# Performance work log

Hardware: AMD Instinct MI355X
Metric: run time of the kernel (lower is better)

The kernel has to match this reference:

```python
import jax, jax.numpy as jnp
import numpy as np

N, E = 100000, 1000000
IN_F, HID, OUT, K = 64, 64, 32, 3


def setup_inputs() -> dict:
    key = jax.random.key(0)
    ks = jax.random.split(key, 8)
    s = 0.05
    return {
        "features": jax.random.normal(ks[0], (N, IN_F), dtype=jnp.float32),
        "src": jax.random.randint(ks[1], (E,), 0, N),
        "dst": jax.random.randint(ks[2], (E,), 0, N),
        "n_nodes": N,
        "W1": jax.random.normal(ks[3], (K * IN_F, HID), jnp.float32) * s,
        "b1": jnp.zeros((HID,), jnp.float32),
        "W2": jax.random.normal(ks[4], (K * HID, HID), jnp.float32) * s,
        "b2": jnp.zeros((HID,), jnp.float32),
        "Wm1": jax.random.normal(ks[5], (HID, HID), jnp.float32) * s,
        "bm1": jnp.zeros((HID,), jnp.float32),
        "Wm2": jax.random.normal(ks[6], (HID, OUT), jnp.float32) * s,
        "bm2": jnp.zeros((OUT,), jnp.float32),
    }


def _cheb_conv(x, src, dst, dinv, W, b, n_nodes, k=K):
    # DGL ChebConv with lambda_max = 2 (re_norm = 2/lambda_max = 1).
    def prop(h):  # D^{-1/2} A D^{-1/2} h via edge gather/scatter
        m = (h * dinv)[src]                                   # [E, F]
        agg = jax.ops.segment_sum(m, dst, num_segments=n_nodes)
        return agg * dinv

    X0 = x
    Xs = [X0]
    X1 = -prop(X0)                 # -re_norm*L h + (re_norm-1)*X0, re_norm=1
    Xs.append(X1)
    for _ in range(2, k):
        Xi = -2.0 * prop(X1) - X0  # Chebyshev recursion
        Xs.append(Xi)
        X0, X1 = X1, Xi
    return jnp.concatenate(Xs, axis=1) @ W + b  # Linear(k*F_in -> F_out)


def reference(features, src, dst, n_nodes, W1, b1, W2, b2, Wm1, bm1, Wm2, bm2):
    deg = jax.ops.segment_sum(
        jnp.ones((src.shape[0],), dtype=features.dtype), dst, num_segments=n_nodes
    )
    dinv = (jnp.clip(deg, 1.0, None) ** -0.5)[:, None]  # in-degree^{-1/2}
    x = jax.nn.relu(_cheb_conv(features, src, dst, dinv, W1, b1, n_nodes))
    x = jax.nn.relu(_cheb_conv(x, src, dst, dinv, W2, b2, n_nodes))
    return jax.nn.relu(x @ Wm1 + bm1) @ Wm2 + bm2
```

## Files before the change

### kernel.cpp

```cpp
#include <hip/hip_runtime.h>


typedef unsigned short ushort_t;
typedef __attribute__((ext_vector_type(8))) short v8s;
typedef __attribute__((ext_vector_type(4))) float v4f;

__device__ inline ushort_t f2bf(float f) {
    unsigned u = __float_as_uint(f);
    return (ushort_t)((u + 0x7FFFu + ((u >> 16) & 1u)) >> 16);
}
__device__ inline float bf2f(ushort_t h) {
    return __uint_as_float(((unsigned)h) << 16);
}

#define BSH 9
#define BSZ (1 << BSH)
#define CHUNK 4096

__global__ void k_wprep(const float* __restrict__ W1, const float* __restrict__ W2,
                        const float* __restrict__ Wm1, const float* __restrict__ Wm2,
                        ushort_t* __restrict__ W1t, ushort_t* __restrict__ W2t,
                        ushort_t* __restrict__ Wm1t, ushort_t* __restrict__ Wm2t,
                        int* __restrict__ gbase, int* __restrict__ done, int NB) {
    int i = blockIdx.x * 256 + threadIdx.x;
    if (i < 12288) { int k = i >> 6, n = i & 63; W1t[n * 192 + k] = f2bf(W1[i]); return; }
    i -= 12288;
    if (i < 12288) { int k = i >> 6, n = i & 63; W2t[n * 192 + k] = f2bf(W2[i]); return; }
    i -= 12288;
    if (i < 4096) { int k = i >> 6, n = i & 63; Wm1t[n * 64 + k] = f2bf(Wm1[i]); return; }
    i -= 4096;
    if (i < 2048) { int k = i >> 5, n = i & 31; Wm2t[n * 64 + k] = f2bf(Wm2[i]); return; }
    i -= 2048;
    if (i < NB) gbase[i] = 0;
    if (i == NB) *done = 0;
}

__global__ __launch_bounds__(256) void k_bhist(const int* __restrict__ dst,
                                               int* __restrict__ gbase,
                                               int* __restrict__ gcur,
                                               int* __restrict__ done, int E, int NB) {
    __shared__ int h[1024];
    __shared__ int isLast;
    for (int i = threadIdx.x; i < NB; i += 256) h[i] = 0;
    __syncthreads();
    for (int i = blockIdx.x * blockDim.x + threadIdx.x; i < E; i += gridDim.x * blockDim.x)
        atomicAdd(&h[dst[i] >> BSH], 1);
    __syncthreads();
    for (int i = threadIdx.x; i < NB; i += 256)
        if (h[i]) atomicAdd(&gbase[i], h[i]);
    __threadfence();
    __syncthreads();
    if (threadIdx.x == 0) isLast = (atomicAdd(done, 1) == (int)gridDim.x - 1);
    __syncthreads();
    if (isLast) {
        __threadfence();
        int t = threadIdx.x;
        int v = (t < NB) ? gbase[t] : 0;
        h[t] = v;
        __syncthreads();
        for (int off = 1; off < 256; off <<= 1) {
            int u = (t >= off) ? h[t - off] : 0;
            __syncthreads();
            h[t] += u;
            __syncthreads();
        }
        if (t < NB) {
            int excl = h[t] - v;
            gbase[t] = excl;
            gcur[t] = excl;
        }
    }
}

__global__ __launch_bounds__(256) void k_bucket2(
    const int* __restrict__ src, const int* __restrict__ dst,
    int* __restrict__ gcur, int2* __restrict__ eb, int E, int NB) {
    __shared__ int ls[CHUNK];
    __shared__ int ld[CHUNK];
    __shared__ int hist[1024];
    __shared__ int bbase[1024];
    int t = threadIdx.x;
    int base = blockIdx.x * CHUNK;
    int count = E - base;
    if (count > CHUNK) count = CHUNK;
    for (int i = t; i < NB; i += 256) hist[i] = 0;
    __syncthreads();
    for (int i = t; i < count; i += 256) {
        int s = src[base + i];
        int d = dst[base + i];
        ls[i] = s;
        ld[i] = d;
        atomicAdd(&hist[d >> BSH], 1);
    }
    __syncthreads();
    for (int b = t; b < NB; b += 256) {
        int c = hist[b];
        bbase[b] = c ? atomicAdd(&gcur[b], c) : 0;
        hist[b] = 0;
    }
    __syncthreads();
    for (int i = t; i < count; i += 256) {
        int d = ld[i];
        int b = d >> BSH;
        int off = atomicAdd(&hist[b], 1);
        eb[bbase[b] + off] = make_int2(ls[i], d);
    }
}

__global__ __launch_bounds__(256) void k_local(
    const int2* __restrict__ eb, const int* __restrict__ gbase,
    int* __restrict__ col, int* __restrict__ row_ptr,
    float* __restrict__ dinv, int N, int E, int NB) {
    __shared__ int cnt[BSZ];
    __shared__ int tsum[256];
    int t = threadIdx.x;
    int b = blockIdx.x;
    int d0 = b << BSH;
    cnt[2 * t] = 0;
    cnt[2 * t + 1] = 0;
    __syncthreads();
    int beg = gbase[b];
    int end = (b + 1 < NB) ? gbase[b + 1] : E;
    for (int i = beg + t; i < end; i += 256)
        atomicAdd(&cnt[eb[i].y - d0], 1);
    __syncthreads();
    int c0 = cnt[2 * t], c1 = cnt[2 * t + 1];
    int mysum = c0 + c1;
    tsum[t] = mysum;
    __syncthreads();
    for (int off = 1; off < 256; off <<= 1) {
        int u = 0;
        if (t >= off) u = tsum[t - off];
        __syncthreads();
        tsum[t] += u;
        __syncthreads();
    }
    int rbase = beg + tsum[t] - mysum;
    int d = d0 + 2 * t;
    if (d < N) {
        row_ptr[d] = rbase;
        dinv[d] = rsqrtf(fmaxf((float)c0, 1.0f));
    }
    if (d + 1 < N) {
        row_ptr[d + 1] = rbase + c0;
        dinv[d + 1] = rsqrtf(fmaxf((float)c1, 1.0f));
    }
    cnt[2 * t] = rbase;
    cnt[2 * t + 1] = rbase + c0;
    __syncthreads();
    for (int i = beg + t; i < end; i += 256) {
        int2 e = eb[i];
        int p = atomicAdd(&cnt[e.y - d0], 1);
        col[p] = e.x;
    }
    if (b == NB - 1 && t == 0) row_ptr[N] = E;
}

__global__ void k_tobf16(const float4* __restrict__ X, const float* __restrict__ dinv,
                         ushort4* __restrict__ Y, int n4) {
    int i = blockIdx.x * blockDim.x + threadIdx.x;
    if (i < n4) {
        float s = dinv[i >> 4];
        float4 v = X[i];
        ushort4 o;
        o.x = f2bf(v.x * s); o.y = f2bf(v.y * s); o.z = f2bf(v.z * s); o.w = f2bf(v.w * s);
        Y[i] = o;
    }
}

__device__ inline float4 gather_sum(const ushort_t* __restrict__ Xb,
                                    const int* __restrict__ col,
                                    int beg, int end, int g, int fl) {
    float4 a0 = make_float4(0.f, 0.f, 0.f, 0.f);
    float4 a1 = make_float4(0.f, 0.f, 0.f, 0.f);
    int e = beg + g;
    for (; e + 4 < end; e += 8) {
        int s0 = col[e], s1 = col[e + 4];
        ushort4 u0 = *(const ushort4*)&Xb[(size_t)s0 * 64 + fl];
        ushort4 u1 = *(const ushort4*)&Xb[(size_t)s1 * 64 + fl];
        a0.x += bf2f(u0.x); a0.y += bf2f(u0.y); a0.z += bf2f(u0.z); a0.w += bf2f(u0.w);
        a1.x += bf2f(u1.x); a1.y += bf2f(u1.y); a1.z += bf2f(u1.z); a1.w += bf2f(u1.w);
    }
    if (e < end) {
        int s0 = col[e];
        ushort4 u0 = *(const ushort4*)&Xb[(size_t)s0 * 64 + fl];
        a0.x += bf2f(u0.x); a0.y += bf2f(u0.y); a0.z += bf2f(u0.z); a0.w += bf2f(u0.w);
    }
    float4 acc;
    acc.x = a0.x + a1.x; acc.y = a0.y + a1.y;
    acc.z = a0.z + a1.z; acc.w = a0.w + a1.w;
    acc.x += __shfl_xor(acc.x, 16); acc.y += __shfl_xor(acc.y, 16);
    acc.z += __shfl_xor(acc.z, 16); acc.w += __shfl_xor(acc.w, 16);
    acc.x += __shfl_xor(acc.x, 32); acc.y += __shfl_xor(acc.y, 32);
    acc.z += __shfl_xor(acc.z, 32); acc.w += __shfl_xor(acc.w, 32);
    return acc;
}

template <int MODE>
__global__ __launch_bounds__(256) void k_prop(
    const ushort_t* __restrict__ Xb, const int* __restrict__ rp,
    const int* __restrict__ col, const float* __restrict__ dinv,
    const ushort_t* __restrict__ X0b, ushort_t* __restrict__ OUTB, int N) {
    int wid = (blockIdx.x * blockDim.x + threadIdx.x) >> 6;
    int lane = threadIdx.x & 63;
    if (wid >= N) return;
    int g = lane >> 4;
    int fl = (lane & 15) * 4;
    int beg = rp[wid], end = rp[wid + 1];
    float4 a0 = make_float4(0.f, 0.f, 0.f, 0.f);
    float4 a1 = make_float4(0.f, 0.f, 0.f, 0.f);
    int e = beg + g;
    for (; e + 4 < end; e += 8) {
        int s0 = col[e], s1 = col[e + 4];
        ushort4 u0 = *(const ushort4*)&Xb[(size_t)s0 * 64 + fl];
        ushort4 u1 = *(const ushort4*)&Xb[(size_t)s1 * 64 + fl];
        a0.x += bf2f(u0.x); a0.y += bf2f(u0.y); a0.z += bf2f(u0.z); a0.w += bf2f(u0.w);
        a1.x += bf2f(u1.x); a1.y += bf2f(u1.y); a1.z += bf2f(u1.z); a1.w += bf2f(u1.w);
    }
    if (e < end) {
        int s0 = col[e];
        ushort4 u0 = *(const ushort4*)&Xb[(size_t)s0 * 64 + fl];
        a0.x += bf2f(u0.x); a0.y += bf2f(u0.y); a0.z += bf2f(u0.z); a0.w += bf2f(u0.w);
    }
    float4 acc;
    acc.x = a0.x + a1.x;
    acc.y = a0.y + a1.y;
    acc.z = a0.z + a1.z;
    acc.w = a0.w + a1.w;
    acc.x += __shfl_xor(acc.x, 16);
    acc.y += __shfl_xor(acc.y, 16);
    acc.z += __shfl_xor(acc.z, 16);
    acc.w += __shfl_xor(acc.w, 16);
    acc.x += __shfl_xor(acc.x, 32);
    acc.y += __shfl_xor(acc.y, 32);
    acc.z += __shfl_xor(acc.z, 32);
    acc.w += __shfl_xor(acc.w, 32);
    if (g == 0) {
        float di = dinv[wid];
        ushort4 ob;
        if (MODE == 1) {
            float m = -di * di;
            ob.x = f2bf(m * acc.x);
            ob.y = f2bf(m * acc.y);
            ob.z = f2bf(m * acc.z);
            ob.w = f2bf(m * acc.w);
        } else {
            ushort4 x0u = *(const ushort4*)&X0b[(size_t)wid * 64 + fl];
            float m = -2.0f * di;
            float rd = 1.0f / di;
            ob.x = f2bf(fmaf(m, acc.x, -rd * bf2f(x0u.x)));
            ob.y = f2bf(fmaf(m, acc.y, -rd * bf2f(x0u.y)));
            ob.z = f2bf(fmaf(m, acc.z, -rd * bf2f(x0u.z)));
            ob.w = f2bf(fmaf(m, acc.w, -rd * bf2f(x0u.w)));
        }
        *(ushort4*)&OUTB[(size_t)wid * 64 + fl] = ob;
    }
}

__global__ __launch_bounds__(512, 8) void k_pc1(
    const ushort_t* __restrict__ Xb, const int* __restrict__ rp,
    const int* __restrict__ col, const float* __restrict__ dinv,
    const ushort_t* __restrict__ T0, const ushort_t* __restrict__ Wt,
    const float* __restrict__ b, ushort_t* __restrict__ Yb, int N) {
    __shared__ ushort_t XA[64][72];
    int tid = threadIdx.x;
    int w = tid >> 6, lane = tid & 63;
    int g = lane >> 4, fl = (lane & 15) * 4;
    int node0 = blockIdx.x * 64;

    for (int i = 0; i < 8; i++) {
        int nd = node0 + w * 8 + i;
        ushort4 ob;
        ob.x = 0; ob.y = 0; ob.z = 0; ob.w = 0;
        if (nd < N) {
            float4 acc = gather_sum(Xb, col, rp[nd], rp[nd + 1], g, fl);
            if (g == 0) {
                float di = dinv[nd];
                ushort4 x0u = *(const ushort4*)&T0[(size_t)nd * 64 + fl];
                float m = -2.0f * di;
                float rd = 1.0f / di;
                ob.x = f2bf(fmaf(m, acc.x, -rd * bf2f(x0u.x)));
                ob.y = f2bf(fmaf(m, acc.y, -rd * bf2f(x0u.y)));
                ob.z = f2bf(fmaf(m, acc.z, -rd * bf2f(x0u.z)));
                ob.w = f2bf(fmaf(m, acc.w, -rd * bf2f(x0u.w)));
            }
        }
        if (g == 0) *(ushort4*)&XA[w * 8 + i][fl] = ob;
    }
    __syncthreads();

    int n16 = lane & 15, q = lane >> 4;
    int f = w >> 1, h = w & 1;
    int arow = node0 + f * 16 + n16;

    v4f acc_s[2], acc_u[2];
    acc_s[0] = (v4f){0.f, 0.f, 0.f, 0.f};
    acc_s[1] = (v4f){0.f, 0.f, 0.f, 0.f};
    acc_u[0] = (v4f){0.f, 0.f, 0.f, 0.f};
    acc_u[1] = (v4f){0.f, 0.f, 0.f, 0.f};
#pragma unroll
    for (int ks = 0; ks < 6; ks++) {
        int c = ks >> 1;
        int kk = (ks & 1) * 32 + q * 8;
        v8s av = {0, 0, 0, 0, 0, 0, 0, 0};
        if (c == 2) {
            av = *(const v8s*)&XA[f * 16 + n16][kk];
        } else {
            const ushort_t* P = (c == 0) ? T0 : Xb;
            if (arow < N) av = *(const v8s*)&P[(size_t)arow * 64 + kk];
        }
#pragma unroll
        for (int t2 = 0; t2 < 2; t2++) {
            int t = h * 2 + t2;
            v8s bv = *(const v8s*)&Wt[(size_t)(t * 16 + n16) * 192 + ks * 32 + q * 8];
            if (c < 2)
                acc_s[t2] = __builtin_amdgcn_mfma_f32_16x16x32_bf16(av, bv, acc_s[t2], 0, 0, 0);
            else
                acc_u[t2] = __builtin_amdgcn_mfma_f32_16x16x32_bf16(av, bv, acc_u[t2], 0, 0, 0);
        }
    }
    int rbase = node0 + f * 16 + q * 4;
#pragma unroll
    for (int r = 0; r < 4; r++) {
        int row = rbase + r;
        if (row < N) {
            float dv = dinv[row];
            float rd = 1.0f / dv;
#pragma unroll
            for (int t2 = 0; t2 < 2; t2++) {
                int t = h * 2 + t2;
                float y = fmaf(rd, acc_s[t2][r], acc_u[t2][r]) + b[t * 16 + n16];
                y = fmaxf(y, 0.0f);
                Yb[(size_t)row * 64 + t * 16 + n16] = f2bf(dv * y);
            }
        }
    }
}

__global__ __launch_bounds__(512, 8) void k_pc2(
    const ushort_t* __restrict__ Xb, const int* __restrict__ rp,
    const int* __restrict__ col, const float* __restrict__ dinv,
    const ushort_t* __restrict__ T0, const ushort_t* __restrict__ Wt,
    const float* __restrict__ b,
    const ushort_t* __restrict__ Wm1t, const float* __restrict__ bm1,
    const ushort_t* __restrict__ Wm2t, const float* __restrict__ bm2,
    float* __restrict__ out, int N) {
    __shared__ ushort_t smem[9728];
    ushort_t (*XA)[72] = (ushort_t(*)[72])smem;
    ushort_t (*Hs0)[76] = (ushort_t(*)[76])smem;
    ushort_t (*Hs1)[76] = (ushort_t(*)[76])(smem + 64 * 76);
    int tid = threadIdx.x;
    int w = tid >> 6, lane = tid & 63;
    int g = lane >> 4, fl = (lane & 15) * 4;
    int node0 = blockIdx.x * 64;

    for (int i = 0; i < 8; i++) {
        int nd = node0 + w * 8 + i;
        ushort4 ob;
        ob.x = 0; ob.y = 0; ob.z = 0; ob.w = 0;
        if (nd < N) {
            float4 acc = gather_sum(Xb, col, rp[nd], rp[nd + 1], g, fl);
            if (g == 0) {
                float di = dinv[nd];
                ushort4 x0u = *(const ushort4*)&T0[(size_t)nd * 64 + fl];
                float m = -2.0f * di;
                float rd = 1.0f / di;
                ob.x = f2bf(fmaf(m, acc.x, -rd * bf2f(x0u.x)));
                ob.y = f2bf(fmaf(m, acc.y, -rd * bf2f(x0u.y)));
                ob.z = f2bf(fmaf(m, acc.z, -rd * bf2f(x0u.z)));
                ob.w = f2bf(fmaf(m, acc.w, -rd * bf2f(x0u.w)));
            }
        }
        if (g == 0) *(ushort4*)&XA[w * 8 + i][fl] = ob;
    }
    __syncthreads();

    int n16 = lane & 15, q = lane >> 4;
    int f = w >> 1, h = w & 1;
    int arow = node0 + f * 16 + n16;

    v8s av4 = *(const v8s*)&XA[f * 16 + n16][q * 8];
    v8s av5 = *(const v8s*)&XA[f * 16 + n16][32 + q * 8];
    __syncthreads();

    v4f acc_s[2], acc_u[2];
    acc_s[0] = (v4f){0.f, 0.f, 0.f, 0.f};
    acc_s[1] = (v4f){0.f, 0.f, 0.f, 0.f};
    acc_u[0] = (v4f){0.f, 0.f, 0.f, 0.f};
    acc_u[1] = (v4f){0.f, 0.f, 0.f, 0.f};
#pragma unroll
    for (int ks = 0; ks < 6; ks++) {
        int c = ks >> 1;
        int kk = (ks & 1) * 32 + q * 8;
        v8s av;
        if (c == 2) {
            av = (ks & 1) ? av5 : av4;
        } else {
            const ushort_t* P = (c == 0) ? T0 : Xb;
            av = (v8s){0, 0, 0, 0, 0, 0, 0, 0};
            if (arow < N) av = *(const v8s*)&P[(size_t)arow * 64 + kk];
        }
#pragma unroll
        for (int t2 = 0; t2 < 2; t2++) {
            int t = h * 2 + t2;
            v8s bv = *(const v8s*)&Wt[(size_t)(t * 16 + n16) * 192 + ks * 32 + q * 8];
            if (c < 2)
                acc_s[t2] = __builtin_amdgcn_mfma_f32_16x16x32_bf16(av, bv, acc_s[t2], 0, 0, 0);
            else
                acc_u[t2] = __builtin_amdgcn_mfma_f32_16x16x32_bf16(av, bv, acc_u[t2], 0, 0, 0);
        }
    }
    int lr = f * 16 + q * 4;
    int rbase = node0 + lr;
#pragma unroll
    for (int r = 0; r < 4; r++) {
        int row = rbase + r;
        if (row < N) {
            float dv = dinv[row];
            float rd = 1.0f / dv;
#pragma unroll
            for (int t2 = 0; t2 < 2; t2++) {
                int t = h * 2 + t2;
                float y = fmaf(rd, acc_s[t2][r], acc_u[t2][r]) + b[t * 16 + n16];
                Hs0[lr + r][t * 16 + n16] = f2bf(fmaxf(y, 0.0f));
            }
        } else {
#pragma unroll
            for (int t2 = 0; t2 < 2; t2++)
                Hs0[lr + r][(h * 2 + t2) * 16 + n16] = 0;
        }
    }
    __syncthreads();

    v4f acc[2];
    acc[0] = (v4f){0.f, 0.f, 0.f, 0.f};
    acc[1] = (v4f){0.f, 0.f, 0.f, 0.f};
#pragma unroll
    for (int ks = 0; ks < 2; ks++) {
        v8s av1 = *(const v8s*)&Hs0[f * 16 + n16][ks * 32 + q * 8];
#pragma unroll
        for (int t2 = 0; t2 < 2; t2++) {
            int t = h * 2 + t2;
            v8s bv = *(const v8s*)&Wm1t[(size_t)(t * 16 + n16) * 64 + ks * 32 + q * 8];
            acc[t2] = __builtin_amdgcn_mfma_f32_16x16x32_bf16(av1, bv, acc[t2], 0, 0, 0);
        }
    }
#pragma unroll
    for (int r = 0; r < 4; r++)
#pragma unroll
        for (int t2 = 0; t2 < 2; t2++) {
            int t = h * 2 + t2;
            float y = acc[t2][r] + bm1[t * 16 + n16];
            Hs1[lr + r][t * 16 + n16] = f2bf(fmaxf(y, 0.0f));
        }
    __syncthreads();

    v4f a2 = (v4f){0.f, 0.f, 0.f, 0.f};
#pragma unroll
    for (int ks = 0; ks < 2; ks++) {
        v8s av2 = *(const v8s*)&Hs1[f * 16 + n16][ks * 32 + q * 8];
        v8s bv = *(const v8s*)&Wm2t[(size_t)(h * 16 + n16) * 64 + ks * 32 + q * 8];
        a2 = __builtin_amdgcn_mfma_f32_16x16x32_bf16(av2, bv, a2, 0, 0, 0);
    }
#pragma unroll
    for (int r = 0; r < 4; r++) {
        int row = rbase + r;
        if (row < N)
            out[(size_t)row * 32 + h * 16 + n16] = a2[r] + bm2[h * 16 + n16];
    }
}

extern "C" void kernel_launch(void* const* d_in, const int* in_sizes, int n_in,
                              void* d_out, int out_size, void* d_ws, size_t ws_size,
                              hipStream_t stream) {
    const float* features = (const float*)d_in[0];
    const int* src = (const int*)d_in[1];
    const int* dst = (const int*)d_in[2];
    const float* W1 = (const float*)d_in[4];
    const float* b1 = (const float*)d_in[5];
    const float* W2 = (const float*)d_in[6];
    const float* b2 = (const float*)d_in[7];
    const float* Wm1 = (const float*)d_in[8];
    const float* bm1 = (const float*)d_in[9];
    const float* Wm2 = (const float*)d_in[10];
    const float* bm2 = (const float*)d_in[11];
    float* out = (float*)d_out;

    int N = in_sizes[0] / 64;
    int E = in_sizes[1];
    int NB = (N + BSZ - 1) >> BSH;

    float* ws = (float*)d_ws;
    float* dinv = ws;
    int* row_ptr = (int*)(dinv + N);
    int* gbase = row_ptr + (N + 1);
    int* gcur = gbase + 1024;
    int* done = gcur + 1024;
    int* col = done + 16;
    int2* eb = (int2*)(((uintptr_t)(col + E) + 7) & ~(uintptr_t)7);
    ushort_t* Fb  = (ushort_t*)(eb + E);
    ushort_t* X1b = Fb  + (size_t)N * 64;
    ushort_t* H1b = X1b + (size_t)N * 64;
    ushort_t* W1t = H1b + (size_t)N * 64;
    ushort_t* W2t = W1t + 64 * 192;
    ushort_t* Wm1t = W2t + 64 * 192;
    ushort_t* Wm2t = Wm1t + 64 * 64;

    int pblk = (N * 64 + 255) / 256;
    int gblk = (N + 63) / 64;
    int n4 = N * 16;
    int cblk = (n4 + 255) / 256;
    int bblk = (E + CHUNK - 1) / CHUNK;

    k_wprep<<<(30720 + 1024 + 255) / 256, 256, 0, stream>>>(
        W1, W2, Wm1, Wm2, W1t, W2t, Wm1t, Wm2t, gbase, done, NB);

    k_bhist<<<512, 256, 0, stream>>>(dst, gbase, gcur, done, E, NB);
    k_bucket2<<<bblk, 256, 0, stream>>>(src, dst, gcur, eb, E, NB);
    k_local<<<NB, 256, 0, stream>>>(eb, gbase, col, row_ptr, dinv, N, E, NB);

    k_tobf16<<<cblk, 256, 0, stream>>>((const float4*)features, dinv, (ushort4*)Fb, n4);

    k_prop<1><<<pblk, 256, 0, stream>>>(Fb, row_ptr, col, dinv, nullptr, X1b, N);
    k_pc1<<<gblk, 512, 0, stream>>>(X1b, row_ptr, col, dinv, Fb, W1t, b1, H1b, N);

    k_prop<1><<<pblk, 256, 0, stream>>>(H1b, row_ptr, col, dinv, nullptr, X1b, N);
    k_pc2<<<gblk, 512, 0, stream>>>(X1b, row_ptr, col, dinv, H1b, W2t, b2,
                                    Wm1t, bm1, Wm2t, bm2, out, N);
}
```

Before: 398.9 us.

## Split bucket scan into separate kernel and preload row pointers in fused convs

The last-block-done prefix scan inside the histogram kernel is replaced by a separate single-block scan kernel launched afterwards, which removes the done counter, the thread fences and the atomic handshake. In the fused propagation+GEMM kernels, the eight nodes' row_ptr begin/end values are loaded up front and the gather loop is unrolled, so the loads are batched rather than serialized inside the loop. This costs one extra kernel launch and more registers in the conv kernels. The new scan also loops up to 1024 lanes, whereas the old one only scanned the first 256 entries.

```diff
diff --git a/kernel.cpp b/kernel.cpp
--- a/kernel.cpp
+++ b/kernel.cpp
@@ -21,7 +21,7 @@
                         const float* __restrict__ Wm1, const float* __restrict__ Wm2,
                         ushort_t* __restrict__ W1t, ushort_t* __restrict__ W2t,
                         ushort_t* __restrict__ Wm1t, ushort_t* __restrict__ Wm2t,
-                        int* __restrict__ gbase, int* __restrict__ done, int NB) {
+                        int* __restrict__ gbase, int NB) {
     int i = blockIdx.x * 256 + threadIdx.x;
     if (i < 12288) { int k = i >> 6, n = i & 63; W1t[n * 192 + k] = f2bf(W1[i]); return; }
     i -= 12288;
@@ -32,15 +32,12 @@
     if (i < 2048) { int k = i >> 5, n = i & 31; Wm2t[n * 64 + k] = f2bf(Wm2[i]); return; }
     i -= 2048;
     if (i < NB) gbase[i] = 0;
-    if (i == NB) *done = 0;
-}
+}
+
 
 __global__ __launch_bounds__(256) void k_bhist(const int* __restrict__ dst,
-                                               int* __restrict__ gbase,
-                                               int* __restrict__ gcur,
-                                               int* __restrict__ done, int E, int NB) {
+                                               int* __restrict__ gbase, int E, int NB) {
     __shared__ int h[1024];
-    __shared__ int isLast;
     for (int i = threadIdx.x; i < NB; i += 256) h[i] = 0;
     __syncthreads();
     for (int i = blockIdx.x * blockDim.x + threadIdx.x; i < E; i += gridDim.x * blockDim.x)
@@ -48,27 +45,25 @@
     __syncthreads();
     for (int i = threadIdx.x; i < NB; i += 256)
         if (h[i]) atomicAdd(&gbase[i], h[i]);
-    __threadfence();
-    __syncthreads();
-    if (threadIdx.x == 0) isLast = (atomicAdd(done, 1) == (int)gridDim.x - 1);
-    __syncthreads();
-    if (isLast) {
-        __threadfence();
-        int t = threadIdx.x;
-        int v = (t < NB) ? gbase[t] : 0;
-        h[t] = v;
+}
+
+__global__ void k_bscan(int* __restrict__ gbase, int* __restrict__ gcur, int NB) {
+    __shared__ int sh[1024];
+    int t = threadIdx.x;
+    int v = (t < NB) ? gbase[t] : 0;
+    sh[t] = v;
+    __syncthreads();
+    for (int off = 1; off < 1024; off <<= 1) {
+        int u = 0;
+        if (t >= off) u = sh[t - off];
         __syncthreads();
-        for (int off = 1; off < 256; off <<= 1) {
-            int u = (t >= off) ? h[t - off] : 0;
-            __syncthreads();
-            h[t] += u;
-            __syncthreads();
-        }
-        if (t < NB) {
-            int excl = h[t] - v;
-            gbase[t] = excl;
-            gcur[t] = excl;
-        }
+        sh[t] += u;
+        __syncthreads();
+    }
+    if (t < NB) {
+        int excl = sh[t] - v;
+        gbase[t] = excl;
+        gcur[t] = excl;
     }
 }
 
@@ -268,12 +263,21 @@
     int g = lane >> 4, fl = (lane & 15) * 4;
     int node0 = blockIdx.x * 64;
 
+    int begs[8], ends[8];
+#pragma unroll
+    for (int i = 0; i < 8; i++) {
+        int nd = node0 + w * 8 + i;
+        begs[i] = (nd < N) ? rp[nd] : 0;
+        ends[i] = (nd < N) ? rp[nd + 1] : 0;
+    }
+
+#pragma unroll
     for (int i = 0; i < 8; i++) {
         int nd = node0 + w * 8 + i;
         ushort4 ob;
         ob.x = 0; ob.y = 0; ob.z = 0; ob.w = 0;
         if (nd < N) {
-            float4 acc = gather_sum(Xb, col, rp[nd], rp[nd + 1], g, fl);
+            float4 acc = gather_sum(Xb, col, begs[i], ends[i], g, fl);
             if (g == 0) {
                 float di = dinv[nd];
                 ushort4 x0u = *(const ushort4*)&T0[(size_t)nd * 64 + fl];
@@ -354,12 +358,21 @@
     int g = lane >> 4, fl = (lane & 15) * 4;
     int node0 = blockIdx.x * 64;
 
+    int begs[8], ends[8];
+#pragma unroll
+    for (int i = 0; i < 8; i++) {
+        int nd = node0 + w * 8 + i;
+        begs[i] = (nd < N) ? rp[nd] : 0;
+        ends[i] = (nd < N) ? rp[nd + 1] : 0;
+    }
+
+#pragma unroll
     for (int i = 0; i < 8; i++) {
         int nd = node0 + w * 8 + i;
         ushort4 ob;
         ob.x = 0; ob.y = 0; ob.z = 0; ob.w = 0;
         if (nd < N) {
-            float4 acc = gather_sum(Xb, col, rp[nd], rp[nd + 1], g, fl);
+            float4 acc = gather_sum(Xb, col, begs[i], ends[i], g, fl);
             if (g == 0) {
                 float di = dinv[nd];
                 ushort4 x0u = *(const ushort4*)&T0[(size_t)nd * 64 + fl];
@@ -495,8 +508,7 @@
     int* row_ptr = (int*)(dinv + N);
     int* gbase = row_ptr + (N + 1);
     int* gcur = gbase + 1024;
-    int* done = gcur + 1024;
-    int* col = done + 16;
+    int* col = gcur + 1024;
     int2* eb = (int2*)(((uintptr_t)(col + E) + 7) & ~(uintptr_t)7);
     ushort_t* Fb  = (ushort_t*)(eb + E);
     ushort_t* X1b = Fb  + (size_t)N * 64;
@@ -513,9 +525,10 @@
     int bblk = (E + CHUNK - 1) / CHUNK;
 
     k_wprep<<<(30720 + 1024 + 255) / 256, 256, 0, stream>>>(
-        W1, W2, Wm1, Wm2, W1t, W2t, Wm1t, Wm2t, gbase, done, NB);
-
-    k_bhist<<<512, 256, 0, stream>>>(dst, gbase, gcur, done, E, NB);
+        W1, W2, Wm1, Wm2, W1t, W2t, Wm1t, Wm2t, gbase, NB);
+
+    k_bhist<<<512, 256, 0, stream>>>(dst, gbase, E, NB);
+    k_bscan<<<1, 1024, 0, stream>>>(gbase, gcur, NB);
     k_bucket2<<<bblk, 256, 0, stream>>>(src, dst, gcur, eb, E, NB);
     k_local<<<NB, 256, 0, stream>>>(eb, gbase, col, row_ptr, dinv, N, E, NB);
 
```

Result: faster. 380.1 us (-4.7%).
